# Optimization experiments

Hardware: AMD Instinct MI355X
Metric: run time of the kernel (lower is better)

The kernel has to match this reference:

```python
import jax, jax.numpy as jnp
import numpy as np

N = 100000      # nodes
E = 1600000     # directed edges (avg degree 16)
D_IN, D_H, D_OUT = 128, 128, 64


def glorot(k, fi, fo):
    s = (6.0 / (fi + fo)) ** 0.5
    return jax.random.uniform(k, (fi, fo), jnp.float32, -s, s)


def setup_inputs() -> dict:
    key = jax.random.key(0)
    ks = jax.random.split(key, 5)
    edges = jax.random.randint(ks[0], (2, E), 0, N)
    features = jax.random.normal(ks[1], (N, D_IN), dtype=jnp.float32)
    return dict(
        edges=edges,
        features=features,
        W0=glorot(ks[2], D_IN, D_H), b0=jnp.zeros((D_H,), jnp.float32),
        W1=glorot(ks[3], D_H, D_H), b1=jnp.zeros((D_H,), jnp.float32),
        W2=glorot(ks[4], D_H, D_OUT), b2=jnp.zeros((D_OUT,), jnp.float32),
    )


def _prep(edges):
    # add self-loops and compute symmetric GCN normalization D^-1/2 A_hat D^-1/2
    loop = jnp.arange(N)
    row = jnp.concatenate([edges[0], loop])  # source
    col = jnp.concatenate([edges[1], loop])  # target
    deg = jax.ops.segment_sum(jnp.ones((row.shape[0],), jnp.float32), col, num_segments=N)
    dinv = jnp.where(deg > 0, jax.lax.rsqrt(deg), 0.0)
    norm = dinv[row] * dinv[col]             # per-edge coefficient
    return row, col, norm


def gcn_conv(x, row, col, norm, W, b):
    x = x @ W                                 # [N, out]
    msg = x[row] * norm[:, None]              # gather + scale, [E+N, out]
    return jax.ops.segment_sum(msg, col, num_segments=N) + b


def reference(edges, features, W0, b0, W1, b1, W2, b2):
    row, col, norm = _prep(edges)
    h = jax.nn.relu(gcn_conv(features, row, col, norm, W0, b0))
    h = jax.nn.relu(gcn_conv(h, row, col, norm, W1, b1))
    h = gcn_conv(h, row, col, norm, W2, b2)
    return jax.nn.log_softmax(h, axis=1)
```

## Files before the change

kernel.cpp:

```cpp
#include <hip/hip_runtime.h>
#include <hip/hip_fp16.h>
#include <math.h>

#define NN 100000
#define EE 1600000
#define NB2 782
#define BN 128
#define NPART 512
#define CAP 2560

typedef __attribute__((ext_vector_type(8))) _Float16 half8;
typedef __attribute__((ext_vector_type(4))) float f32x4;
typedef __attribute__((ext_vector_type(4))) unsigned int u32x4;

__device__ inline unsigned short f2h(float x) {
    return __half_as_ushort(__float2half(x));
}
__device__ inline __half2 u2h2(unsigned u) {
    return __builtin_bit_cast(__half2, u);
}
__device__ inline unsigned h22u(__half2 h) {
    return __builtin_bit_cast(unsigned, h);
}


__global__ __launch_bounds__(256) void scatter_bump(const int* __restrict__ src,
                                                    const int* __restrict__ dst,
                                                    int* __restrict__ bcount,
                                                    int* __restrict__ P, int e,
                                                    const float* __restrict__ W0,
                                                    const float* __restrict__ W1,
                                                    const float* __restrict__ W2,
                                                    unsigned short* __restrict__ Wt0,
                                                    unsigned short* __restrict__ Wt1,
                                                    unsigned short* __restrict__ Wt2) {
    __shared__ int cnt[NB2];
    __shared__ int basep[NB2];
    __shared__ int cur[NB2];
    int t = threadIdx.x;
    {
        int g = blockIdx.x * 256 + t;
        if (g < 16384) {
            int n = g >> 7, k = g & 127;
            Wt0[g] = f2h(W0[k * 128 + n]);
        } else if (g < 32768) {
            int i = g - 16384;
            int n = i >> 7, k = i & 127;
            Wt1[i] = f2h(W1[k * 128 + n]);
        } else if (g < 40960) {
            int i = g - 32768;
            int n = i >> 7, k = i & 127;
            Wt2[i] = f2h(W2[k * 64 + n]);
        }
    }
    for (int i = t; i < NB2; i += 256) { cnt[i] = 0; cur[i] = 0; }
    __syncthreads();
    int chunk = (e + NPART - 1) / NPART;
    int b0 = blockIdx.x * chunk, b1 = min(e, b0 + chunk);
    for (int i = b0 + t; i < b1; i += 256)
        atomicAdd(&cnt[dst[i] >> 7], 1);
    __syncthreads();
    for (int i = t; i < NB2; i += 256) {
        int c = cnt[i];
        basep[i] = c ? atomicAdd(&bcount[i], c) : 0;
    }
    __syncthreads();
    for (int i = b0 + t; i < b1; i += 256) {
        int d = dst[i];
        int b = d >> 7;
        int p = basep[b] + atomicAdd(&cur[b], 1);
        P[(size_t)b * CAP + p] = (src[i] << 7) | (d & 127);
    }
}

__global__ __launch_bounds__(256) void bucket_build(const int* __restrict__ P,
                                                    const int* __restrict__ bcount,
                                                    int2* __restrict__ offs2,
                                                    float* __restrict__ dinv,
                                                    int* __restrict__ csr, int n) {
    __shared__ int cnt[BN];
    __shared__ int sc[BN];
    __shared__ int cur[BN];
    __shared__ int stage[CAP];
    int b = blockIdx.x, t = threadIdx.x;
    int base = b * CAP;
    int count = bcount[b];
    if (t < BN) cnt[t] = 0;
    __syncthreads();
    for (int i = t; i < count; i += 256)
        atomicAdd(&cnt[P[base + i] & 127], 1);
    __syncthreads();
    int v = 0;
    if (t < BN) {
        v = cnt[t];
        sc[t] = v;
    }
    for (int d = 1; d < BN; d <<= 1) {
        __syncthreads();
        int x = (t < BN && t >= d) ? sc[t - d] : 0;
        __syncthreads();
        if (t < BN) sc[t] += x;
    }
    __syncthreads();
    if (t < BN) {
        int myoff = sc[t] - v;
        int node = b * BN + t;
        if (node < n) {
            offs2[node] = make_int2(base + myoff, base + myoff + v);
            dinv[node] = 1.0f / sqrtf((float)(v + 1));
        }
        cur[t] = myoff;
    }
    __syncthreads();
    for (int i = t; i < count; i += 256) {
        int pe = P[base + i];
        int p = atomicAdd(&cur[pe & 127], 1);
        stage[p] = ((unsigned)pe) >> 7;
    }
    __syncthreads();
    for (int i = t; i < count; i += 256) csr[base + i] = stage[i];
}

__device__ inline half8 load_xrow_f32(const float* A, int row, int col, int nrows) {
    if (row >= nrows) {
        u32x4 z = {0u, 0u, 0u, 0u};
        return __builtin_bit_cast(half8, z);
    }
    const float* p = A + (size_t)row * 128 + col;
    float4 v0 = *(const float4*)p;
    float4 v1 = *(const float4*)(p + 4);
    u32x4 u;
    u.x = h22u(__floats2half2_rn(v0.x, v0.y));
    u.y = h22u(__floats2half2_rn(v0.z, v0.w));
    u.z = h22u(__floats2half2_rn(v1.x, v1.y));
    u.w = h22u(__floats2half2_rn(v1.z, v1.w));
    return __builtin_bit_cast(half8, u);
}

__global__ __launch_bounds__(256) void gemm0_mfma(const float* __restrict__ Aptr,
                                                  const unsigned short* __restrict__ Wt,
                                                  const float* __restrict__ dinv,
                                                  unsigned short* __restrict__ Y, int nrows) {
    constexpr int KP = 136;
    constexpr int NT = 8;
    __shared__ unsigned short sW[128 * KP];
    const int row0 = blockIdx.x * 128;
    const int tid = threadIdx.x;

    for (int i = tid; i < 128 * 16; i += 256) {
        int n = i >> 4, c = (i & 15) * 8;
        *(uint4*)(&sW[n * KP + c]) = *(const uint4*)(Wt + n * 128 + c);
    }
    __syncthreads();

    const int wave = tid >> 6;
    const int lane = tid & 63;
    const int m0 = lane & 15;
    const int kq = (lane >> 4) * 8;
    const int xr0 = row0 + wave * 32 + m0;
    const int xr1 = xr0 + 16;

    f32x4 acc[2][NT];
#pragma unroll
    for (int rt = 0; rt < 2; ++rt)
#pragma unroll
        for (int t = 0; t < NT; ++t) acc[rt][t] = (f32x4){0.f, 0.f, 0.f, 0.f};

#pragma unroll
    for (int k0 = 0; k0 < 128; k0 += 32) {
        half8 b0 = load_xrow_f32(Aptr, xr0, k0 + kq, nrows);
        half8 b1 = load_xrow_f32(Aptr, xr1, k0 + kq, nrows);
#pragma unroll
        for (int t = 0; t < NT; ++t) {
            half8 aW = *(const half8*)(&sW[(t * 16 + m0) * KP + k0 + kq]);
            acc[0][t] = __builtin_amdgcn_mfma_f32_16x16x32_f16(aW, b0, acc[0][t], 0, 0, 0);
            acc[1][t] = __builtin_amdgcn_mfma_f32_16x16x32_f16(aW, b1, acc[1][t], 0, 0, 0);
        }
    }

#pragma unroll
    for (int rt = 0; rt < 2; ++rt) {
        int xrow = row0 + wave * 32 + rt * 16 + m0;
        if (xrow < nrows) {
            float dv = dinv[xrow];
#pragma unroll
            for (int t = 0; t < NT; ++t) {
                uint2 o;
                o.x = h22u(__floats2half2_rn(acc[rt][t][0] * dv, acc[rt][t][1] * dv));
                o.y = h22u(__floats2half2_rn(acc[rt][t][2] * dv, acc[rt][t][3] * dv));
                *(uint2*)(Y + (size_t)xrow * 128 + t * 16 + (lane >> 4) * 4) = o;
            }
        }
    }
}

template <int DOUT>
__global__ __launch_bounds__(256) void agg_gemm(const unsigned short* __restrict__ Xg,
                                                const int* __restrict__ csr,
                                                const int2* __restrict__ offs2,
                                                const float* __restrict__ dinv,
                                                const float* __restrict__ biasPrev,
                                                const unsigned short* __restrict__ Wt,
                                                unsigned short* __restrict__ Y, int n) {
    constexpr int KP = 136;
    constexpr int NT = DOUT / 16;
    __shared__ unsigned short sX[128 * KP];
    __shared__ unsigned short sW[DOUT * KP];
    const int row0 = blockIdx.x * 128;
    const int tid = threadIdx.x;

    for (int i = tid; i < DOUT * 16; i += 256) {
        int nn = i >> 4, c = (i & 15) * 8;
        *(uint4*)(&sW[nn * KP + c]) = *(const uint4*)(Wt + nn * 128 + c);
    }

    const int g = tid >> 4;
    const int l = tid & 15;
    const unsigned short* __restrict__ Xl = Xg + l * 8;
    const float4 bA = *(const float4*)(biasPrev + l * 8);
    const float4 bB = *(const float4*)(biasPrev + l * 8 + 4);
    const __half2 hz = __floats2half2_rn(0.f, 0.f);

    for (int sub = 0; sub < 8; ++sub) {
        const int local = sub * 16 + g;
        const int node = row0 + local;
        uint4 o = make_uint4(0u, 0u, 0u, 0u);
        if (node < n) {
            int2 se = offs2[node];
            int s = se.x, deg = se.y - se.x;
            __half2 aA0 = hz, aA1 = hz, aA2 = hz, aA3 = hz;
            __half2 aB0 = hz, aB1 = hz, aB2 = hz, aB3 = hz;
            int j = 0;
            for (; j + 8 <= deg; j += 8) {
                int i0 = csr[s + j],     i1 = csr[s + j + 1], i2 = csr[s + j + 2], i3 = csr[s + j + 3];
                int i4 = csr[s + j + 4], i5 = csr[s + j + 5], i6 = csr[s + j + 6], i7 = csr[s + j + 7];
                uint4 u0 = *(const uint4*)(Xl + (size_t)i0 * 128);
                uint4 u1 = *(const uint4*)(Xl + (size_t)i1 * 128);
                uint4 u2 = *(const uint4*)(Xl + (size_t)i2 * 128);
                uint4 u3 = *(const uint4*)(Xl + (size_t)i3 * 128);
                uint4 u4 = *(const uint4*)(Xl + (size_t)i4 * 128);
                uint4 u5 = *(const uint4*)(Xl + (size_t)i5 * 128);
                uint4 u6 = *(const uint4*)(Xl + (size_t)i6 * 128);
                uint4 u7 = *(const uint4*)(Xl + (size_t)i7 * 128);
                aA0 = __hadd2(aA0, u2h2(u0.x)); aA1 = __hadd2(aA1, u2h2(u0.y));
                aA2 = __hadd2(aA2, u2h2(u0.z)); aA3 = __hadd2(aA3, u2h2(u0.w));
                aB0 = __hadd2(aB0, u2h2(u1.x)); aB1 = __hadd2(aB1, u2h2(u1.y));
                aB2 = __hadd2(aB2, u2h2(u1.z)); aB3 = __hadd2(aB3, u2h2(u1.w));
                aA0 = __hadd2(aA0, u2h2(u2.x)); aA1 = __hadd2(aA1, u2h2(u2.y));
                aA2 = __hadd2(aA2, u2h2(u2.z)); aA3 = __hadd2(aA3, u2h2(u2.w));
                aB0 = __hadd2(aB0, u2h2(u3.x)); aB1 = __hadd2(aB1, u2h2(u3.y));
                aB2 = __hadd2(aB2, u2h2(u3.z)); aB3 = __hadd2(aB3, u2h2(u3.w));
                aA0 = __hadd2(aA0, u2h2(u4.x)); aA1 = __hadd2(aA1, u2h2(u4.y));
                aA2 = __hadd2(aA2, u2h2(u4.z)); aA3 = __hadd2(aA3, u2h2(u4.w));
                aB0 = __hadd2(aB0, u2h2(u5.x)); aB1 = __hadd2(aB1, u2h2(u5.y));
                aB2 = __hadd2(aB2, u2h2(u5.z)); aB3 = __hadd2(aB3, u2h2(u5.w));
                aA0 = __hadd2(aA0, u2h2(u6.x)); aA1 = __hadd2(aA1, u2h2(u6.y));
                aA2 = __hadd2(aA2, u2h2(u6.z)); aA3 = __hadd2(aA3, u2h2(u6.w));
                aB0 = __hadd2(aB0, u2h2(u7.x)); aB1 = __hadd2(aB1, u2h2(u7.y));
                aB2 = __hadd2(aB2, u2h2(u7.z)); aB3 = __hadd2(aB3, u2h2(u7.w));
            }
            for (; j < deg; ++j) {
                int i0 = csr[s + j];
                uint4 u = *(const uint4*)(Xl + (size_t)i0 * 128);
                aA0 = __hadd2(aA0, u2h2(u.x)); aA1 = __hadd2(aA1, u2h2(u.y));
                aA2 = __hadd2(aA2, u2h2(u.z)); aA3 = __hadd2(aA3, u2h2(u.w));
            }
            {
                uint4 u = *(const uint4*)(Xl + (size_t)node * 128);
                aB0 = __hadd2(aB0, u2h2(u.x)); aB1 = __hadd2(aB1, u2h2(u.y));
                aB2 = __hadd2(aB2, u2h2(u.z)); aB3 = __hadd2(aB3, u2h2(u.w));
            }
            float di = dinv[node];
            float2 fA, fB;
            fA = __half22float2(aA0); fB = __half22float2(aB0);
            float r0 = fA.x + fB.x, r1 = fA.y + fB.y;
            fA = __half22float2(aA1); fB = __half22float2(aB1);
            float r2 = fA.x + fB.x, r3 = fA.y + fB.y;
            fA = __half22float2(aA2); fB = __half22float2(aB2);
            float r4 = fA.x + fB.x, r5 = fA.y + fB.y;
            fA = __half22float2(aA3); fB = __half22float2(aB3);
            float r6 = fA.x + fB.x, r7 = fA.y + fB.y;
            r0 = fmaxf(fmaf(di, r0, bA.x), 0.f); r1 = fmaxf(fmaf(di, r1, bA.y), 0.f);
            r2 = fmaxf(fmaf(di, r2, bA.z), 0.f); r3 = fmaxf(fmaf(di, r3, bA.w), 0.f);
            r4 = fmaxf(fmaf(di, r4, bB.x), 0.f); r5 = fmaxf(fmaf(di, r5, bB.y), 0.f);
            r6 = fmaxf(fmaf(di, r6, bB.z), 0.f); r7 = fmaxf(fmaf(di, r7, bB.w), 0.f);
            o.x = h22u(__floats2half2_rn(r0, r1));
            o.y = h22u(__floats2half2_rn(r2, r3));
            o.z = h22u(__floats2half2_rn(r4, r5));
            o.w = h22u(__floats2half2_rn(r6, r7));
        }
        *(uint4*)(&sX[local * KP + l * 8]) = o;
    }
    __syncthreads();

    const int wave = tid >> 6;
    const int lane = tid & 63;
    const int m0 = lane & 15;
    const int kq = (lane >> 4) * 8;

    f32x4 acc[2][NT];
#pragma unroll
    for (int rt = 0; rt < 2; ++rt)
#pragma unroll
        for (int t = 0; t < NT; ++t) acc[rt][t] = (f32x4){0.f, 0.f, 0.f, 0.f};

#pragma unroll
    for (int k0 = 0; k0 < 128; k0 += 32) {
        half8 b0 = *(const half8*)(&sX[(wave * 32 + m0) * KP + k0 + kq]);
        half8 b1 = *(const half8*)(&sX[(wave * 32 + 16 + m0) * KP + k0 + kq]);
#pragma unroll
        for (int t = 0; t < NT; ++t) {
            half8 aW = *(const half8*)(&sW[(t * 16 + m0) * KP + k0 + kq]);
            acc[0][t] = __builtin_amdgcn_mfma_f32_16x16x32_f16(aW, b0, acc[0][t], 0, 0, 0);
            acc[1][t] = __builtin_amdgcn_mfma_f32_16x16x32_f16(aW, b1, acc[1][t], 0, 0, 0);
        }
    }

#pragma unroll
    for (int rt = 0; rt < 2; ++rt) {
        int xrow = row0 + wave * 32 + rt * 16 + m0;
        if (xrow < n) {
            float dv = dinv[xrow];
#pragma unroll
            for (int t = 0; t < NT; ++t) {
                uint2 o;
                o.x = h22u(__floats2half2_rn(acc[rt][t][0] * dv, acc[rt][t][1] * dv));
                o.y = h22u(__floats2half2_rn(acc[rt][t][2] * dv, acc[rt][t][3] * dv));
                *(uint2*)(Y + (size_t)xrow * DOUT + t * 16 + (lane >> 4) * 4) = o;
            }
        }
    }
}

__global__ __launch_bounds__(256) void agg_softmax64_f16(const unsigned short* __restrict__ Xp,
                                                         const int* __restrict__ csr,
                                                         const int2* __restrict__ offs2,
                                                         const float* __restrict__ dinv,
                                                         const float* __restrict__ bias,
                                                         float* __restrict__ out, int n) {
    const int tid = threadIdx.x;
    const int node = blockIdx.x * 32 + (tid >> 3);
    if (node >= n) return;
    const int l = tid & 7;
    const unsigned short* __restrict__ Xl = Xp + l * 8;

    int2 se = offs2[node];
    int s = se.x, deg = se.y - se.x;
    const __half2 hz = __floats2half2_rn(0.f, 0.f);
    __half2 aA0 = hz, aA1 = hz, aA2 = hz, aA3 = hz;
    __half2 aB0 = hz, aB1 = hz, aB2 = hz, aB3 = hz;
    int j = 0;
    for (; j + 8 <= deg; j += 8) {
        int i0 = csr[s + j],     i1 = csr[s + j + 1], i2 = csr[s + j + 2], i3 = csr[s + j + 3];
        int i4 = csr[s + j + 4], i5 = csr[s + j + 5], i6 = csr[s + j + 6], i7 = csr[s + j + 7];
        uint4 u0 = *(const uint4*)(Xl + (size_t)i0 * 64);
        uint4 u1 = *(const uint4*)(Xl + (size_t)i1 * 64);
        uint4 u2 = *(const uint4*)(Xl + (size_t)i2 * 64);
        uint4 u3 = *(const uint4*)(Xl + (size_t)i3 * 64);
        uint4 u4 = *(const uint4*)(Xl + (size_t)i4 * 64);
        uint4 u5 = *(const uint4*)(Xl + (size_t)i5 * 64);
        uint4 u6 = *(const uint4*)(Xl + (size_t)i6 * 64);
        uint4 u7 = *(const uint4*)(Xl + (size_t)i7 * 64);
        aA0 = __hadd2(aA0, u2h2(u0.x)); aA1 = __hadd2(aA1, u2h2(u0.y));
        aA2 = __hadd2(aA2, u2h2(u0.z)); aA3 = __hadd2(aA3, u2h2(u0.w));
        aB0 = __hadd2(aB0, u2h2(u1.x)); aB1 = __hadd2(aB1, u2h2(u1.y));
        aB2 = __hadd2(aB2, u2h2(u1.z)); aB3 = __hadd2(aB3, u2h2(u1.w));
        aA0 = __hadd2(aA0, u2h2(u2.x)); aA1 = __hadd2(aA1, u2h2(u2.y));
        aA2 = __hadd2(aA2, u2h2(u2.z)); aA3 = __hadd2(aA3, u2h2(u2.w));
        aB0 = __hadd2(aB0, u2h2(u3.x)); aB1 = __hadd2(aB1, u2h2(u3.y));
        aB2 = __hadd2(aB2, u2h2(u3.z)); aB3 = __hadd2(aB3, u2h2(u3.w));
        aA0 = __hadd2(aA0, u2h2(u4.x)); aA1 = __hadd2(aA1, u2h2(u4.y));
        aA2 = __hadd2(aA2, u2h2(u4.z)); aA3 = __hadd2(aA3, u2h2(u4.w));
        aB0 = __hadd2(aB0, u2h2(u5.x)); aB1 = __hadd2(aB1, u2h2(u5.y));
        aB2 = __hadd2(aB2, u2h2(u5.z)); aB3 = __hadd2(aB3, u2h2(u5.w));
        aA0 = __hadd2(aA0, u2h2(u6.x)); aA1 = __hadd2(aA1, u2h2(u6.y));
        aA2 = __hadd2(aA2, u2h2(u6.z)); aA3 = __hadd2(aA3, u2h2(u6.w));
        aB0 = __hadd2(aB0, u2h2(u7.x)); aB1 = __hadd2(aB1, u2h2(u7.y));
        aB2 = __hadd2(aB2, u2h2(u7.z)); aB3 = __hadd2(aB3, u2h2(u7.w));
    }
    for (; j < deg; ++j) {
        int i0 = csr[s + j];
        uint4 u = *(const uint4*)(Xl + (size_t)i0 * 64);
        aA0 = __hadd2(aA0, u2h2(u.x)); aA1 = __hadd2(aA1, u2h2(u.y));
        aA2 = __hadd2(aA2, u2h2(u.z)); aA3 = __hadd2(aA3, u2h2(u.w));
    }
    {
        uint4 u = *(const uint4*)(Xl + (size_t)node * 64);
        aB0 = __hadd2(aB0, u2h2(u.x)); aB1 = __hadd2(aB1, u2h2(u.y));
        aB2 = __hadd2(aB2, u2h2(u.z)); aB3 = __hadd2(aB3, u2h2(u.w));
    }
    float di = dinv[node];
    float4 bA = *(const float4*)(bias + l * 8);
    float4 bB = *(const float4*)(bias + l * 8 + 4);
    float2 fA, fB;
    fA = __half22float2(aA0); fB = __half22float2(aB0);
    float r0 = fA.x + fB.x, r1 = fA.y + fB.y;
    fA = __half22float2(aA1); fB = __half22float2(aB1);
    float r2 = fA.x + fB.x, r3 = fA.y + fB.y;
    fA = __half22float2(aA2); fB = __half22float2(aB2);
    float r4 = fA.x + fB.x, r5 = fA.y + fB.y;
    fA = __half22float2(aA3); fB = __half22float2(aB3);
    float r6 = fA.x + fB.x, r7 = fA.y + fB.y;
    r0 = fmaf(di, r0, bA.x); r1 = fmaf(di, r1, bA.y);
    r2 = fmaf(di, r2, bA.z); r3 = fmaf(di, r3, bA.w);
    r4 = fmaf(di, r4, bB.x); r5 = fmaf(di, r5, bB.y);
    r6 = fmaf(di, r6, bB.z); r7 = fmaf(di, r7, bB.w);
    float m = fmaxf(fmaxf(fmaxf(r0, r1), fmaxf(r2, r3)), fmaxf(fmaxf(r4, r5), fmaxf(r6, r7)));
    m = fmaxf(m, __shfl_xor(m, 1));
    m = fmaxf(m, __shfl_xor(m, 2));
    m = fmaxf(m, __shfl_xor(m, 4));
    float ssum = __expf(r0 - m) + __expf(r1 - m) + __expf(r2 - m) + __expf(r3 - m) +
                 __expf(r4 - m) + __expf(r5 - m) + __expf(r6 - m) + __expf(r7 - m);
    ssum += __shfl_xor(ssum, 1);
    ssum += __shfl_xor(ssum, 2);
    ssum += __shfl_xor(ssum, 4);
    float lg = m + __logf(ssum);
    float4 o0 = make_float4(r0 - lg, r1 - lg, r2 - lg, r3 - lg);
    float4 o1 = make_float4(r4 - lg, r5 - lg, r6 - lg, r7 - lg);
    *(float4*)(out + (size_t)node * 64 + l * 8) = o0;
    *(float4*)(out + (size_t)node * 64 + l * 8 + 4) = o1;
}


extern "C" void kernel_launch(void* const* d_in, const int* in_sizes, int n_in,
                              void* d_out, int out_size, void* d_ws, size_t ws_size,
                              hipStream_t stream) {
    const int* edges = (const int*)d_in[0];
    const float* feat = (const float*)d_in[1];
    const float* W0 = (const float*)d_in[2];
    const float* b0 = (const float*)d_in[3];
    const float* W1 = (const float*)d_in[4];
    const float* b1 = (const float*)d_in[5];
    const float* W2 = (const float*)d_in[6];
    const float* b2 = (const float*)d_in[7];

    const int N = NN;
    const int E = EE;

    char* ws = (char*)d_ws;
    int* bcount = (int*)ws;
    int2* offs2 = (int2*)(bcount + ((NB2 + 1) & ~1));
    float* dinv = (float*)(offs2 + N);
    int* P = (int*)(dinv + N);
    int* csr = P + (size_t)NB2 * CAP;
    unsigned short* Wt0 = (unsigned short*)(csr + (size_t)NB2 * CAP);
    unsigned short* Wt1 = Wt0 + 16384;
    unsigned short* Wt2 = Wt1 + 16384;
    size_t off = (size_t)((char*)(Wt2 + 8192) - ws);
    off = (off + 255) & ~(size_t)255;
    unsigned short* bufA = (unsigned short*)(ws + off);
    unsigned short* bufB = bufA + (size_t)N * 128;

    const int* esrc = edges;
    const int* edst = edges + E;

    hipMemsetAsync(bcount, 0, NB2 * sizeof(int), stream);
    scatter_bump<<<NPART, 256, 0, stream>>>(esrc, edst, bcount, P, E,
                                            W0, W1, W2, Wt0, Wt1, Wt2);
    bucket_build<<<NB2, 256, 0, stream>>>(P, bcount, offs2, dinv, csr, N);

    const int gemmBlocks = (N + 127) / 128;
    const int aggsmBlocks = (N + 31) / 32;

    gemm0_mfma<<<gemmBlocks, 256, 0, stream>>>(feat, Wt0, dinv, bufA, N);
    agg_gemm<128><<<gemmBlocks, 256, 0, stream>>>(bufA, csr, offs2, dinv, b0, Wt1, bufB, N);
    agg_gemm<64><<<gemmBlocks, 256, 0, stream>>>(bufB, csr, offs2, dinv, b1, Wt2, bufA, N);
    agg_softmax64_f16<<<aggsmBlocks, 256, 0, stream>>>(bufA, csr, offs2, dinv, b2, (float*)d_out, N);
}
```

Measured before the change: 419.6 us.

## Aggregate directly into MFMA register fragments, dropping shared-memory staging

The fused aggregate+GEMM kernel now has each lane gather neighbor rows straight into the register layout the MFMA B operand needs. This removes the shared-memory X and W tiles and the block barrier, and W fragments are read straight from global/L2. Each lane now handles 2 rows with 4 uint4 loads per neighbor, unrolled by 2 instead of 8. Launch bounds ask for 4 blocks per CU to raise occupancy. The risks are less memory-level parallelism per lane, more redundant W loads, and different fp16 summation order.

Result: faster. 379.8 us (-9.5%).

```diff
diff --git a/kernel.cpp b/kernel.cpp
--- a/kernel.cpp
+++ b/kernel.cpp
@@ -21,6 +21,14 @@
 }
 __device__ inline unsigned h22u(__half2 h) {
     return __builtin_bit_cast(unsigned, h);
+}
+__device__ inline uint4 h4add(uint4 a, uint4 b) {
+    uint4 r;
+    r.x = h22u(__hadd2(u2h2(a.x), u2h2(b.x)));
+    r.y = h22u(__hadd2(u2h2(a.y), u2h2(b.y)));
+    r.z = h22u(__hadd2(u2h2(a.z), u2h2(b.z)));
+    r.w = h22u(__hadd2(u2h2(a.w), u2h2(b.w)));
+    return r;
 }
 
 
@@ -194,140 +202,139 @@
     }
 }
 
+
+__device__ inline void agg_row_frag(const unsigned short* __restrict__ Xg,
+                                    const int* __restrict__ csr,
+                                    int2 se, int node, int kq,
+                                    uint4& c0, uint4& c1, uint4& c2, uint4& c3) {
+    int s = se.x, deg = se.y - se.x;
+    int j = 0;
+    for (; j + 2 <= deg; j += 2) {
+        int i0 = csr[s + j], i1 = csr[s + j + 1];
+        const unsigned short* p0 = Xg + (size_t)i0 * 128 + kq;
+        const unsigned short* p1 = Xg + (size_t)i1 * 128 + kq;
+        uint4 a0 = *(const uint4*)(p0);
+        uint4 a1 = *(const uint4*)(p0 + 32);
+        uint4 a2 = *(const uint4*)(p0 + 64);
+        uint4 a3 = *(const uint4*)(p0 + 96);
+        uint4 b0 = *(const uint4*)(p1);
+        uint4 b1 = *(const uint4*)(p1 + 32);
+        uint4 b2 = *(const uint4*)(p1 + 64);
+        uint4 b3 = *(const uint4*)(p1 + 96);
+        c0 = h4add(c0, h4add(a0, b0));
+        c1 = h4add(c1, h4add(a1, b1));
+        c2 = h4add(c2, h4add(a2, b2));
+        c3 = h4add(c3, h4add(a3, b3));
+    }
+    if (j < deg) {
+        int i0 = csr[s + j];
+        const unsigned short* p0 = Xg + (size_t)i0 * 128 + kq;
+        c0 = h4add(c0, *(const uint4*)(p0));
+        c1 = h4add(c1, *(const uint4*)(p0 + 32));
+        c2 = h4add(c2, *(const uint4*)(p0 + 64));
+        c3 = h4add(c3, *(const uint4*)(p0 + 96));
+    }
+    {
+        const unsigned short* p0 = Xg + (size_t)node * 128 + kq;
+        c0 = h4add(c0, *(const uint4*)(p0));
+        c1 = h4add(c1, *(const uint4*)(p0 + 32));
+        c2 = h4add(c2, *(const uint4*)(p0 + 64));
+        c3 = h4add(c3, *(const uint4*)(p0 + 96));
+    }
+}
+
+__device__ inline half8 finish_frag(uint4 c, float di, const float* __restrict__ bias, int coff) {
+    float4 ba = *(const float4*)(bias + coff);
+    float4 bb = *(const float4*)(bias + coff + 4);
+    float2 f;
+    f = __half22float2(u2h2(c.x));
+    float r0 = fmaxf(fmaf(di, f.x, ba.x), 0.f), r1 = fmaxf(fmaf(di, f.y, ba.y), 0.f);
+    f = __half22float2(u2h2(c.y));
+    float r2 = fmaxf(fmaf(di, f.x, ba.z), 0.f), r3 = fmaxf(fmaf(di, f.y, ba.w), 0.f);
+    f = __half22float2(u2h2(c.z));
+    float r4 = fmaxf(fmaf(di, f.x, bb.x), 0.f), r5 = fmaxf(fmaf(di, f.y, bb.y), 0.f);
+    f = __half22float2(u2h2(c.w));
+    float r6 = fmaxf(fmaf(di, f.x, bb.z), 0.f), r7 = fmaxf(fmaf(di, f.y, bb.w), 0.f);
+    u32x4 o;
+    o.x = h22u(__floats2half2_rn(r0, r1));
+    o.y = h22u(__floats2half2_rn(r2, r3));
+    o.z = h22u(__floats2half2_rn(r4, r5));
+    o.w = h22u(__floats2half2_rn(r6, r7));
+    return __builtin_bit_cast(half8, o);
+}
+
 template <int DOUT>
-__global__ __launch_bounds__(256) void agg_gemm(const unsigned short* __restrict__ Xg,
+__global__ __launch_bounds__(256, 4) void aggmm(const unsigned short* __restrict__ Xg,
                                                 const int* __restrict__ csr,
                                                 const int2* __restrict__ offs2,
                                                 const float* __restrict__ dinv,
                                                 const float* __restrict__ biasPrev,
                                                 const unsigned short* __restrict__ Wt,
                                                 unsigned short* __restrict__ Y, int n) {
-    constexpr int KP = 136;
     constexpr int NT = DOUT / 16;
-    __shared__ unsigned short sX[128 * KP];
-    __shared__ unsigned short sW[DOUT * KP];
-    const int row0 = blockIdx.x * 128;
     const int tid = threadIdx.x;
-
-    for (int i = tid; i < DOUT * 16; i += 256) {
-        int nn = i >> 4, c = (i & 15) * 8;
-        *(uint4*)(&sW[nn * KP + c]) = *(const uint4*)(Wt + nn * 128 + c);
-    }
-
-    const int g = tid >> 4;
-    const int l = tid & 15;
-    const unsigned short* __restrict__ Xl = Xg + l * 8;
-    const float4 bA = *(const float4*)(biasPrev + l * 8);
-    const float4 bB = *(const float4*)(biasPrev + l * 8 + 4);
-    const __half2 hz = __floats2half2_rn(0.f, 0.f);
-
-    for (int sub = 0; sub < 8; ++sub) {
-        const int local = sub * 16 + g;
-        const int node = row0 + local;
-        uint4 o = make_uint4(0u, 0u, 0u, 0u);
-        if (node < n) {
-            int2 se = offs2[node];
-            int s = se.x, deg = se.y - se.x;
-            __half2 aA0 = hz, aA1 = hz, aA2 = hz, aA3 = hz;
-            __half2 aB0 = hz, aB1 = hz, aB2 = hz, aB3 = hz;
-            int j = 0;
-            for (; j + 8 <= deg; j += 8) {
-                int i0 = csr[s + j],     i1 = csr[s + j + 1], i2 = csr[s + j + 2], i3 = csr[s + j + 3];
-                int i4 = csr[s + j + 4], i5 = csr[s + j + 5], i6 = csr[s + j + 6], i7 = csr[s + j + 7];
-                uint4 u0 = *(const uint4*)(Xl + (size_t)i0 * 128);
-                uint4 u1 = *(const uint4*)(Xl + (size_t)i1 * 128);
-                uint4 u2 = *(const uint4*)(Xl + (size_t)i2 * 128);
-                uint4 u3 = *(const uint4*)(Xl + (size_t)i3 * 128);
-                uint4 u4 = *(const uint4*)(Xl + (size_t)i4 * 128);
-                uint4 u5 = *(const uint4*)(Xl + (size_t)i5 * 128);
-                uint4 u6 = *(const uint4*)(Xl + (size_t)i6 * 128);
-                uint4 u7 = *(const uint4*)(Xl + (size_t)i7 * 128);
-                aA0 = __hadd2(aA0, u2h2(u0.x)); aA1 = __hadd2(aA1, u2h2(u0.y));
-                aA2 = __hadd2(aA2, u2h2(u0.z)); aA3 = __hadd2(aA3, u2h2(u0.w));
-                aB0 = __hadd2(aB0, u2h2(u1.x)); aB1 = __hadd2(aB1, u2h2(u1.y));
-                aB2 = __hadd2(aB2, u2h2(u1.z)); aB3 = __hadd2(aB3, u2h2(u1.w));
-                aA0 = __hadd2(aA0, u2h2(u2.x)); aA1 = __hadd2(aA1, u2h2(u2.y));
-                aA2 = __hadd2(aA2, u2h2(u2.z)); aA3 = __hadd2(aA3, u2h2(u2.w));
-                aB0 = __hadd2(aB0, u2h2(u3.x)); aB1 = __hadd2(aB1, u2h2(u3.y));
-                aB2 = __hadd2(aB2, u2h2(u3.z)); aB3 = __hadd2(aB3, u2h2(u3.w));
-                aA0 = __hadd2(aA0, u2h2(u4.x)); aA1 = __hadd2(aA1, u2h2(u4.y));
-                aA2 = __hadd2(aA2, u2h2(u4.z)); aA3 = __hadd2(aA3, u2h2(u4.w));
-                aB0 = __hadd2(aB0, u2h2(u5.x)); aB1 = __hadd2(aB1, u2h2(u5.y));
-                aB2 = __hadd2(aB2, u2h2(u5.z)); aB3 = __hadd2(aB3, u2h2(u5.w));
-                aA0 = __hadd2(aA0, u2h2(u6.x)); aA1 = __hadd2(aA1, u2h2(u6.y));
-                aA2 = __hadd2(aA2, u2h2(u6.z)); aA3 = __hadd2(aA3, u2h2(u6.w));
-                aB0 = __hadd2(aB0, u2h2(u7.x)); aB1 = __hadd2(aB1, u2h2(u7.y));
-                aB2 = __hadd2(aB2, u2h2(u7.z)); aB3 = __hadd2(aB3, u2h2(u7.w));
-            }
-            for (; j < deg; ++j) {
-                int i0 = csr[s + j];
-                uint4 u = *(const uint4*)(Xl + (size_t)i0 * 128);
-                aA0 = __hadd2(aA0, u2h2(u.x)); aA1 = __hadd2(aA1, u2h2(u.y));
-                aA2 = __hadd2(aA2, u2h2(u.z)); aA3 = __hadd2(aA3, u2h2(u.w));
-            }
-            {
-                uint4 u = *(const uint4*)(Xl + (size_t)node * 128);
-                aB0 = __hadd2(aB0, u2h2(u.x)); aB1 = __hadd2(aB1, u2h2(u.y));
-                aB2 = __hadd2(aB2, u2h2(u.z)); aB3 = __hadd2(aB3, u2h2(u.w));
-            }
-            float di = dinv[node];
-            float2 fA, fB;
-            fA = __half22float2(aA0); fB = __half22float2(aB0);
-            float r0 = fA.x + fB.x, r1 = fA.y + fB.y;
-            fA = __half22float2(aA1); fB = __half22float2(aB1);
-            float r2 = fA.x + fB.x, r3 = fA.y + fB.y;
-            fA = __half22float2(aA2); fB = __half22float2(aB2);
-            float r4 = fA.x + fB.x, r5 = fA.y + fB.y;
-            fA = __half22float2(aA3); fB = __half22float2(aB3);
-            float r6 = fA.x + fB.x, r7 = fA.y + fB.y;
-            r0 = fmaxf(fmaf(di, r0, bA.x), 0.f); r1 = fmaxf(fmaf(di, r1, bA.y), 0.f);
-            r2 = fmaxf(fmaf(di, r2, bA.z), 0.f); r3 = fmaxf(fmaf(di, r3, bA.w), 0.f);
-            r4 = fmaxf(fmaf(di, r4, bB.x), 0.f); r5 = fmaxf(fmaf(di, r5, bB.y), 0.f);
-            r6 = fmaxf(fmaf(di, r6, bB.z), 0.f); r7 = fmaxf(fmaf(di, r7, bB.w), 0.f);
-            o.x = h22u(__floats2half2_rn(r0, r1));
-            o.y = h22u(__floats2half2_rn(r2, r3));
-            o.z = h22u(__floats2half2_rn(r4, r5));
-            o.w = h22u(__floats2half2_rn(r6, r7));
-        }
-        *(uint4*)(&sX[local * KP + l * 8]) = o;
-    }
-    __syncthreads();
-
     const int wave = tid >> 6;
     const int lane = tid & 63;
     const int m0 = lane & 15;
     const int kq = (lane >> 4) * 8;
-
-    f32x4 acc[2][NT];
-#pragma unroll
-    for (int rt = 0; rt < 2; ++rt)
-#pragma unroll
-        for (int t = 0; t < NT; ++t) acc[rt][t] = (f32x4){0.f, 0.f, 0.f, 0.f};
-
-#pragma unroll
-    for (int k0 = 0; k0 < 128; k0 += 32) {
-        half8 b0 = *(const half8*)(&sX[(wave * 32 + m0) * KP + k0 + kq]);
-        half8 b1 = *(const half8*)(&sX[(wave * 32 + 16 + m0) * KP + k0 + kq]);
-#pragma unroll
-        for (int t = 0; t < NT; ++t) {
-            half8 aW = *(const half8*)(&sW[(t * 16 + m0) * KP + k0 + kq]);
-            acc[0][t] = __builtin_amdgcn_mfma_f32_16x16x32_f16(aW, b0, acc[0][t], 0, 0, 0);
-            acc[1][t] = __builtin_amdgcn_mfma_f32_16x16x32_f16(aW, b1, acc[1][t], 0, 0, 0);
-        }
-    }
-
-#pragma unroll
-    for (int rt = 0; rt < 2; ++rt) {
-        int xrow = row0 + wave * 32 + rt * 16 + m0;
-        if (xrow < n) {
-            float dv = dinv[xrow];
-#pragma unroll
-            for (int t = 0; t < NT; ++t) {
-                uint2 o;
-                o.x = h22u(__floats2half2_rn(acc[rt][t][0] * dv, acc[rt][t][1] * dv));
-                o.y = h22u(__floats2half2_rn(acc[rt][t][2] * dv, acc[rt][t][3] * dv));
-                *(uint2*)(Y + (size_t)xrow * DOUT + t * 16 + (lane >> 4) * 4) = o;
-            }
+    const int row0 = blockIdx.x * 128;
+    const int rA = row0 + wave * 32 + m0;
+    const int rB = rA + 16;
+
+    const uint4 z4 = make_uint4(0u, 0u, 0u, 0u);
+    uint4 cA0 = z4, cA1 = z4, cA2 = z4, cA3 = z4;
+    uint4 cB0 = z4, cB1 = z4, cB2 = z4, cB3 = z4;
+    if (rA < n) agg_row_frag(Xg, csr, offs2[rA], rA, kq, cA0, cA1, cA2, cA3);
+    if (rB < n) agg_row_frag(Xg, csr, offs2[rB], rB, kq, cB0, cB1, cB2, cB3);
+
+    const u32x4 z8 = {0u, 0u, 0u, 0u};
+    const half8 hz8 = __builtin_bit_cast(half8, z8);
+    float diA = 0.f, diB = 0.f;
+    half8 fA0 = hz8, fA1 = hz8, fA2 = hz8, fA3 = hz8;
+    half8 fB0 = hz8, fB1 = hz8, fB2 = hz8, fB3 = hz8;
+    if (rA < n) {
+        diA = dinv[rA];
+        fA0 = finish_frag(cA0, diA, biasPrev, 0 + kq);
+        fA1 = finish_frag(cA1, diA, biasPrev, 32 + kq);
+        fA2 = finish_frag(cA2, diA, biasPrev, 64 + kq);
+        fA3 = finish_frag(cA3, diA, biasPrev, 96 + kq);
+    }
+    if (rB < n) {
+        diB = dinv[rB];
+        fB0 = finish_frag(cB0, diB, biasPrev, 0 + kq);
+        fB1 = finish_frag(cB1, diB, biasPrev, 32 + kq);
+        fB2 = finish_frag(cB2, diB, biasPrev, 64 + kq);
+        fB3 = finish_frag(cB3, diB, biasPrev, 96 + kq);
+    }
+
+#pragma unroll
+    for (int t = 0; t < NT; ++t) {
+        const unsigned short* wp = Wt + (size_t)(t * 16 + m0) * 128 + kq;
+        half8 w0 = *(const half8*)(wp);
+        half8 w1 = *(const half8*)(wp + 32);
+        half8 w2 = *(const half8*)(wp + 64);
+        half8 w3 = *(const half8*)(wp + 96);
+        f32x4 q0 = (f32x4){0.f, 0.f, 0.f, 0.f};
+        f32x4 q1 = (f32x4){0.f, 0.f, 0.f, 0.f};
+        q0 = __builtin_amdgcn_mfma_f32_16x16x32_f16(w0, fA0, q0, 0, 0, 0);
+        q1 = __builtin_amdgcn_mfma_f32_16x16x32_f16(w0, fB0, q1, 0, 0, 0);
+        q0 = __builtin_amdgcn_mfma_f32_16x16x32_f16(w1, fA1, q0, 0, 0, 0);
+        q1 = __builtin_amdgcn_mfma_f32_16x16x32_f16(w1, fB1, q1, 0, 0, 0);
+        q0 = __builtin_amdgcn_mfma_f32_16x16x32_f16(w2, fA2, q0, 0, 0, 0);
+        q1 = __builtin_amdgcn_mfma_f32_16x16x32_f16(w2, fB2, q1, 0, 0, 0);
+        q0 = __builtin_amdgcn_mfma_f32_16x16x32_f16(w3, fA3, q0, 0, 0, 0);
+        q1 = __builtin_amdgcn_mfma_f32_16x16x32_f16(w3, fB3, q1, 0, 0, 0);
+        if (rA < n) {
+            uint2 o;
+            o.x = h22u(__floats2half2_rn(q0[0] * diA, q0[1] * diA));
+            o.y = h22u(__floats2half2_rn(q0[2] * diA, q0[3] * diA));
+            *(uint2*)(Y + (size_t)rA * DOUT + t * 16 + (lane >> 4) * 4) = o;
+        }
+        if (rB < n) {
+            uint2 o;
+            o.x = h22u(__floats2half2_rn(q1[0] * diB, q1[1] * diB));
+            o.y = h22u(__floats2half2_rn(q1[2] * diB, q1[3] * diB));
+            *(uint2*)(Y + (size_t)rB * DOUT + t * 16 + (lane >> 4) * 4) = o;
         }
     }
 }
@@ -463,7 +470,7 @@
     const int aggsmBlocks = (N + 31) / 32;
 
     gemm0_mfma<<<gemmBlocks, 256, 0, stream>>>(feat, Wt0, dinv, bufA, N);
-    agg_gemm<128><<<gemmBlocks, 256, 0, stream>>>(bufA, csr, offs2, dinv, b0, Wt1, bufB, N);
-    agg_gemm<64><<<gemmBlocks, 256, 0, stream>>>(bufB, csr, offs2, dinv, b1, Wt2, bufA, N);
+    aggmm<128><<<gemmBlocks, 256, 0, stream>>>(bufA, csr, offs2, dinv, b0, Wt1, bufB, N);
+    aggmm<64><<<gemmBlocks, 256, 0, stream>>>(bufB, csr, offs2, dinv, b1, Wt2, bufA, N);
     agg_softmax64_f16<<<aggsmBlocks, 256, 0, stream>>>(bufA, csr, offs2, dinv, b2, (float*)d_out, N);
 }
```

## Shrink fused aggregate-GEMM blocks to 16 nodes and read weights from global

Applied to the files above, without the earlier changes.

The fused aggregation+GEMM kernel now processes 16 nodes per block instead of 128. Each thread gathers one node once instead of looping over 8 sub-tiles, and the weight tile is no longer staged in shared memory. Each wave instead loads its slice of W directly from global/L2 and runs one 16-row MFMA tile. Shared memory per block drops from about 70KB to about 4KB, which should allow more resident blocks and more memory-level parallelism in the gather. The cost is redundant weight reads per block, and the code drops bounds checks because it relies on N being divisible by 16.

After: 355.3 us. -15.3%, faster.

```diff
diff --git a/kernel.cpp b/kernel.cpp
--- a/kernel.cpp
+++ b/kernel.cpp
@@ -195,101 +195,90 @@
 }
 
 template <int DOUT>
-__global__ __launch_bounds__(256) void agg_gemm(const unsigned short* __restrict__ Xg,
-                                                const int* __restrict__ csr,
-                                                const int2* __restrict__ offs2,
-                                                const float* __restrict__ dinv,
-                                                const float* __restrict__ biasPrev,
-                                                const unsigned short* __restrict__ Wt,
-                                                unsigned short* __restrict__ Y, int n) {
+__global__ __launch_bounds__(256) void aggmm_blk(const unsigned short* __restrict__ Xg,
+                                                 const int* __restrict__ csr,
+                                                 const int2* __restrict__ offs2,
+                                                 const float* __restrict__ dinv,
+                                                 const float* __restrict__ biasPrev,
+                                                 const unsigned short* __restrict__ Wt,
+                                                 unsigned short* __restrict__ Y, int n) {
     constexpr int KP = 136;
     constexpr int NT = DOUT / 16;
-    __shared__ unsigned short sX[128 * KP];
-    __shared__ unsigned short sW[DOUT * KP];
-    const int row0 = blockIdx.x * 128;
+    constexpr int TPW = NT / 4;
+    __shared__ unsigned short sX[16 * KP];
     const int tid = threadIdx.x;
 
-    for (int i = tid; i < DOUT * 16; i += 256) {
-        int nn = i >> 4, c = (i & 15) * 8;
-        *(uint4*)(&sW[nn * KP + c]) = *(const uint4*)(Wt + nn * 128 + c);
-    }
-
-    const int g = tid >> 4;
-    const int l = tid & 15;
-    const unsigned short* __restrict__ Xl = Xg + l * 8;
-    const float4 bA = *(const float4*)(biasPrev + l * 8);
-    const float4 bB = *(const float4*)(biasPrev + l * 8 + 4);
-    const __half2 hz = __floats2half2_rn(0.f, 0.f);
-
-    for (int sub = 0; sub < 8; ++sub) {
-        const int local = sub * 16 + g;
-        const int node = row0 + local;
-        uint4 o = make_uint4(0u, 0u, 0u, 0u);
-        if (node < n) {
-            int2 se = offs2[node];
-            int s = se.x, deg = se.y - se.x;
-            __half2 aA0 = hz, aA1 = hz, aA2 = hz, aA3 = hz;
-            __half2 aB0 = hz, aB1 = hz, aB2 = hz, aB3 = hz;
-            int j = 0;
-            for (; j + 8 <= deg; j += 8) {
-                int i0 = csr[s + j],     i1 = csr[s + j + 1], i2 = csr[s + j + 2], i3 = csr[s + j + 3];
-                int i4 = csr[s + j + 4], i5 = csr[s + j + 5], i6 = csr[s + j + 6], i7 = csr[s + j + 7];
-                uint4 u0 = *(const uint4*)(Xl + (size_t)i0 * 128);
-                uint4 u1 = *(const uint4*)(Xl + (size_t)i1 * 128);
-                uint4 u2 = *(const uint4*)(Xl + (size_t)i2 * 128);
-                uint4 u3 = *(const uint4*)(Xl + (size_t)i3 * 128);
-                uint4 u4 = *(const uint4*)(Xl + (size_t)i4 * 128);
-                uint4 u5 = *(const uint4*)(Xl + (size_t)i5 * 128);
-                uint4 u6 = *(const uint4*)(Xl + (size_t)i6 * 128);
-                uint4 u7 = *(const uint4*)(Xl + (size_t)i7 * 128);
-                aA0 = __hadd2(aA0, u2h2(u0.x)); aA1 = __hadd2(aA1, u2h2(u0.y));
-                aA2 = __hadd2(aA2, u2h2(u0.z)); aA3 = __hadd2(aA3, u2h2(u0.w));
-                aB0 = __hadd2(aB0, u2h2(u1.x)); aB1 = __hadd2(aB1, u2h2(u1.y));
-                aB2 = __hadd2(aB2, u2h2(u1.z)); aB3 = __hadd2(aB3, u2h2(u1.w));
-                aA0 = __hadd2(aA0, u2h2(u2.x)); aA1 = __hadd2(aA1, u2h2(u2.y));
-                aA2 = __hadd2(aA2, u2h2(u2.z)); aA3 = __hadd2(aA3, u2h2(u2.w));
-                aB0 = __hadd2(aB0, u2h2(u3.x)); aB1 = __hadd2(aB1, u2h2(u3.y));
-                aB2 = __hadd2(aB2, u2h2(u3.z)); aB3 = __hadd2(aB3, u2h2(u3.w));
-                aA0 = __hadd2(aA0, u2h2(u4.x)); aA1 = __hadd2(aA1, u2h2(u4.y));
-                aA2 = __hadd2(aA2, u2h2(u4.z)); aA3 = __hadd2(aA3, u2h2(u4.w));
-                aB0 = __hadd2(aB0, u2h2(u5.x)); aB1 = __hadd2(aB1, u2h2(u5.y));
-                aB2 = __hadd2(aB2, u2h2(u5.z)); aB3 = __hadd2(aB3, u2h2(u5.w));
-                aA0 = __hadd2(aA0, u2h2(u6.x)); aA1 = __hadd2(aA1, u2h2(u6.y));
-                aA2 = __hadd2(aA2, u2h2(u6.z)); aA3 = __hadd2(aA3, u2h2(u6.w));
-                aB0 = __hadd2(aB0, u2h2(u7.x)); aB1 = __hadd2(aB1, u2h2(u7.y));
-                aB2 = __hadd2(aB2, u2h2(u7.z)); aB3 = __hadd2(aB3, u2h2(u7.w));
-            }
-            for (; j < deg; ++j) {
-                int i0 = csr[s + j];
-                uint4 u = *(const uint4*)(Xl + (size_t)i0 * 128);
-                aA0 = __hadd2(aA0, u2h2(u.x)); aA1 = __hadd2(aA1, u2h2(u.y));
-                aA2 = __hadd2(aA2, u2h2(u.z)); aA3 = __hadd2(aA3, u2h2(u.w));
-            }
-            {
-                uint4 u = *(const uint4*)(Xl + (size_t)node * 128);
-                aB0 = __hadd2(aB0, u2h2(u.x)); aB1 = __hadd2(aB1, u2h2(u.y));
-                aB2 = __hadd2(aB2, u2h2(u.z)); aB3 = __hadd2(aB3, u2h2(u.w));
-            }
-            float di = dinv[node];
-            float2 fA, fB;
-            fA = __half22float2(aA0); fB = __half22float2(aB0);
-            float r0 = fA.x + fB.x, r1 = fA.y + fB.y;
-            fA = __half22float2(aA1); fB = __half22float2(aB1);
-            float r2 = fA.x + fB.x, r3 = fA.y + fB.y;
-            fA = __half22float2(aA2); fB = __half22float2(aB2);
-            float r4 = fA.x + fB.x, r5 = fA.y + fB.y;
-            fA = __half22float2(aA3); fB = __half22float2(aB3);
-            float r6 = fA.x + fB.x, r7 = fA.y + fB.y;
-            r0 = fmaxf(fmaf(di, r0, bA.x), 0.f); r1 = fmaxf(fmaf(di, r1, bA.y), 0.f);
-            r2 = fmaxf(fmaf(di, r2, bA.z), 0.f); r3 = fmaxf(fmaf(di, r3, bA.w), 0.f);
-            r4 = fmaxf(fmaf(di, r4, bB.x), 0.f); r5 = fmaxf(fmaf(di, r5, bB.y), 0.f);
-            r6 = fmaxf(fmaf(di, r6, bB.z), 0.f); r7 = fmaxf(fmaf(di, r7, bB.w), 0.f);
-            o.x = h22u(__floats2half2_rn(r0, r1));
-            o.y = h22u(__floats2half2_rn(r2, r3));
-            o.z = h22u(__floats2half2_rn(r4, r5));
-            o.w = h22u(__floats2half2_rn(r6, r7));
-        }
-        *(uint4*)(&sX[local * KP + l * 8]) = o;
+    {
+        const int node = blockIdx.x * 16 + (tid >> 4);
+        const int l = tid & 15;
+        const unsigned short* __restrict__ Xl = Xg + l * 8;
+        int2 se = offs2[node];
+        int s = se.x, deg = se.y - se.x;
+        const __half2 hz = __floats2half2_rn(0.f, 0.f);
+        __half2 aA0 = hz, aA1 = hz, aA2 = hz, aA3 = hz;
+        __half2 aB0 = hz, aB1 = hz, aB2 = hz, aB3 = hz;
+        int j = 0;
+        for (; j + 8 <= deg; j += 8) {
+            int i0 = csr[s + j],     i1 = csr[s + j + 1], i2 = csr[s + j + 2], i3 = csr[s + j + 3];
+            int i4 = csr[s + j + 4], i5 = csr[s + j + 5], i6 = csr[s + j + 6], i7 = csr[s + j + 7];
+            uint4 u0 = *(const uint4*)(Xl + (size_t)i0 * 128);
+            uint4 u1 = *(const uint4*)(Xl + (size_t)i1 * 128);
+            uint4 u2 = *(const uint4*)(Xl + (size_t)i2 * 128);
+            uint4 u3 = *(const uint4*)(Xl + (size_t)i3 * 128);
+            uint4 u4 = *(const uint4*)(Xl + (size_t)i4 * 128);
+            uint4 u5 = *(const uint4*)(Xl + (size_t)i5 * 128);
+            uint4 u6 = *(const uint4*)(Xl + (size_t)i6 * 128);
+            uint4 u7 = *(const uint4*)(Xl + (size_t)i7 * 128);
+            aA0 = __hadd2(aA0, u2h2(u0.x)); aA1 = __hadd2(aA1, u2h2(u0.y));
+            aA2 = __hadd2(aA2, u2h2(u0.z)); aA3 = __hadd2(aA3, u2h2(u0.w));
+            aB0 = __hadd2(aB0, u2h2(u1.x)); aB1 = __hadd2(aB1, u2h2(u1.y));
+            aB2 = __hadd2(aB2, u2h2(u1.z)); aB3 = __hadd2(aB3, u2h2(u1.w));
+            aA0 = __hadd2(aA0, u2h2(u2.x)); aA1 = __hadd2(aA1, u2h2(u2.y));
+            aA2 = __hadd2(aA2, u2h2(u2.z)); aA3 = __hadd2(aA3, u2h2(u2.w));
+            aB0 = __hadd2(aB0, u2h2(u3.x)); aB1 = __hadd2(aB1, u2h2(u3.y));
+            aB2 = __hadd2(aB2, u2h2(u3.z)); aB3 = __hadd2(aB3, u2h2(u3.w));
+            aA0 = __hadd2(aA0, u2h2(u4.x)); aA1 = __hadd2(aA1, u2h2(u4.y));
+            aA2 = __hadd2(aA2, u2h2(u4.z)); aA3 = __hadd2(aA3, u2h2(u4.w));
+            aB0 = __hadd2(aB0, u2h2(u5.x)); aB1 = __hadd2(aB1, u2h2(u5.y));
+            aB2 = __hadd2(aB2, u2h2(u5.z)); aB3 = __hadd2(aB3, u2h2(u5.w));
+            aA0 = __hadd2(aA0, u2h2(u6.x)); aA1 = __hadd2(aA1, u2h2(u6.y));
+            aA2 = __hadd2(aA2, u2h2(u6.z)); aA3 = __hadd2(aA3, u2h2(u6.w));
+            aB0 = __hadd2(aB0, u2h2(u7.x)); aB1 = __hadd2(aB1, u2h2(u7.y));
+            aB2 = __hadd2(aB2, u2h2(u7.z)); aB3 = __hadd2(aB3, u2h2(u7.w));
+        }
+        for (; j < deg; ++j) {
+            int i0 = csr[s + j];
+            uint4 u = *(const uint4*)(Xl + (size_t)i0 * 128);
+            aA0 = __hadd2(aA0, u2h2(u.x)); aA1 = __hadd2(aA1, u2h2(u.y));
+            aA2 = __hadd2(aA2, u2h2(u.z)); aA3 = __hadd2(aA3, u2h2(u.w));
+        }
+        {
+            uint4 u = *(const uint4*)(Xl + (size_t)node * 128);
+            aB0 = __hadd2(aB0, u2h2(u.x)); aB1 = __hadd2(aB1, u2h2(u.y));
+            aB2 = __hadd2(aB2, u2h2(u.z)); aB3 = __hadd2(aB3, u2h2(u.w));
+        }
+        float di = dinv[node];
+        float4 bA = *(const float4*)(biasPrev + l * 8);
+        float4 bB = *(const float4*)(biasPrev + l * 8 + 4);
+        float2 fA, fB;
+        fA = __half22float2(aA0); fB = __half22float2(aB0);
+        float r0 = fA.x + fB.x, r1 = fA.y + fB.y;
+        fA = __half22float2(aA1); fB = __half22float2(aB1);
+        float r2 = fA.x + fB.x, r3 = fA.y + fB.y;
+        fA = __half22float2(aA2); fB = __half22float2(aB2);
+        float r4 = fA.x + fB.x, r5 = fA.y + fB.y;
+        fA = __half22float2(aA3); fB = __half22float2(aB3);
+        float r6 = fA.x + fB.x, r7 = fA.y + fB.y;
+        r0 = fmaxf(fmaf(di, r0, bA.x), 0.f); r1 = fmaxf(fmaf(di, r1, bA.y), 0.f);
+        r2 = fmaxf(fmaf(di, r2, bA.z), 0.f); r3 = fmaxf(fmaf(di, r3, bA.w), 0.f);
+        r4 = fmaxf(fmaf(di, r4, bB.x), 0.f); r5 = fmaxf(fmaf(di, r5, bB.y), 0.f);
+        r6 = fmaxf(fmaf(di, r6, bB.z), 0.f); r7 = fmaxf(fmaf(di, r7, bB.w), 0.f);
+        uint4 o;
+        o.x = h22u(__floats2half2_rn(r0, r1));
+        o.y = h22u(__floats2half2_rn(r2, r3));
+        o.z = h22u(__floats2half2_rn(r4, r5));
+        o.w = h22u(__floats2half2_rn(r6, r7));
+        *(uint4*)(&sX[(tid >> 4) * KP + l * 8]) = o;
     }
     __syncthreads();
 
@@ -297,38 +286,31 @@
     const int lane = tid & 63;
     const int m0 = lane & 15;
     const int kq = (lane >> 4) * 8;
-
-    f32x4 acc[2][NT];
-#pragma unroll
-    for (int rt = 0; rt < 2; ++rt)
-#pragma unroll
-        for (int t = 0; t < NT; ++t) acc[rt][t] = (f32x4){0.f, 0.f, 0.f, 0.f};
-
-#pragma unroll
-    for (int k0 = 0; k0 < 128; k0 += 32) {
-        half8 b0 = *(const half8*)(&sX[(wave * 32 + m0) * KP + k0 + kq]);
-        half8 b1 = *(const half8*)(&sX[(wave * 32 + 16 + m0) * KP + k0 + kq]);
-#pragma unroll
-        for (int t = 0; t < NT; ++t) {
-            half8 aW = *(const half8*)(&sW[(t * 16 + m0) * KP + k0 + kq]);
-            acc[0][t] = __builtin_amdgcn_mfma_f32_16x16x32_f16(aW, b0, acc[0][t], 0, 0, 0);
-            acc[1][t] = __builtin_amdgcn_mfma_f32_16x16x32_f16(aW, b1, acc[1][t], 0, 0, 0);
-        }
-    }
-
-#pragma unroll
-    for (int rt = 0; rt < 2; ++rt) {
-        int xrow = row0 + wave * 32 + rt * 16 + m0;
-        if (xrow < n) {
-            float dv = dinv[xrow];
-#pragma unroll
-            for (int t = 0; t < NT; ++t) {
-                uint2 o;
-                o.x = h22u(__floats2half2_rn(acc[rt][t][0] * dv, acc[rt][t][1] * dv));
-                o.y = h22u(__floats2half2_rn(acc[rt][t][2] * dv, acc[rt][t][3] * dv));
-                *(uint2*)(Y + (size_t)xrow * DOUT + t * 16 + (lane >> 4) * 4) = o;
-            }
-        }
+    const int row = blockIdx.x * 16 + m0;
+    const float dv = dinv[row];
+
+    half8 b0 = *(const half8*)(&sX[m0 * KP + 0 + kq]);
+    half8 b1 = *(const half8*)(&sX[m0 * KP + 32 + kq]);
+    half8 b2 = *(const half8*)(&sX[m0 * KP + 64 + kq]);
+    half8 b3 = *(const half8*)(&sX[m0 * KP + 96 + kq]);
+
+#pragma unroll
+    for (int tt = 0; tt < TPW; ++tt) {
+        const int t = wave * TPW + tt;
+        const unsigned short* wp = Wt + (size_t)(t * 16 + m0) * 128 + kq;
+        half8 w0 = *(const half8*)(wp);
+        half8 w1 = *(const half8*)(wp + 32);
+        half8 w2 = *(const half8*)(wp + 64);
+        half8 w3 = *(const half8*)(wp + 96);
+        f32x4 q = (f32x4){0.f, 0.f, 0.f, 0.f};
+        q = __builtin_amdgcn_mfma_f32_16x16x32_f16(w0, b0, q, 0, 0, 0);
+        q = __builtin_amdgcn_mfma_f32_16x16x32_f16(w1, b1, q, 0, 0, 0);
+        q = __builtin_amdgcn_mfma_f32_16x16x32_f16(w2, b2, q, 0, 0, 0);
+        q = __builtin_amdgcn_mfma_f32_16x16x32_f16(w3, b3, q, 0, 0, 0);
+        uint2 o;
+        o.x = h22u(__floats2half2_rn(q[0] * dv, q[1] * dv));
+        o.y = h22u(__floats2half2_rn(q[2] * dv, q[3] * dv));
+        *(uint2*)(Y + (size_t)row * DOUT + t * 16 + (lane >> 4) * 4) = o;
     }
 }
 
@@ -460,10 +442,11 @@
     bucket_build<<<NB2, 256, 0, stream>>>(P, bcount, offs2, dinv, csr, N);
 
     const int gemmBlocks = (N + 127) / 128;
+    const int fuseBlocks = N / 16;
     const int aggsmBlocks = (N + 31) / 32;
 
     gemm0_mfma<<<gemmBlocks, 256, 0, stream>>>(feat, Wt0, dinv, bufA, N);
-    agg_gemm<128><<<gemmBlocks, 256, 0, stream>>>(bufA, csr, offs2, dinv, b0, Wt1, bufB, N);
-    agg_gemm<64><<<gemmBlocks, 256, 0, stream>>>(bufB, csr, offs2, dinv, b1, Wt2, bufA, N);
+    aggmm_blk<128><<<fuseBlocks, 256, 0, stream>>>(bufA, csr, offs2, dinv, b0, Wt1, bufB, N);
+    aggmm_blk<64><<<fuseBlocks, 256, 0, stream>>>(bufB, csr, offs2, dinv, b1, Wt2, bufA, N);
     agg_softmax64_f16<<<aggsmBlocks, 256, 0, stream>>>(bufA, csr, offs2, dinv, b2, (float*)d_out, N);
 }
```
